# Kernel optimization log

Hardware: AMD Instinct MI355X
Metric: run time of the kernel (lower is better)

The kernel has to match this reference:

```python
import jax, jax.numpy as jnp
import numpy as np

B, T, D, H = 2, 2048, 1024, 16
DH = D // H
TOPK = 64


def setup_inputs() -> dict:
    key = jax.random.key(0)
    ks = jax.random.split(key, 10)
    s = D ** -0.5
    x = jax.random.normal(ks[0], (B, T, D), dtype=jnp.float32)
    key_padding_mask = jax.random.bernoulli(ks[1], 0.1, (B, T))
    Wq = jax.random.normal(ks[2], (D, D), dtype=jnp.float32) * s
    bq = jnp.zeros((D,), dtype=jnp.float32)
    Wk = jax.random.normal(ks[3], (D, D), dtype=jnp.float32) * s
    bk = jnp.zeros((D,), dtype=jnp.float32)
    Wv = jax.random.normal(ks[4], (D, D), dtype=jnp.float32) * s
    bv = jnp.zeros((D,), dtype=jnp.float32)
    Wo = jax.random.normal(ks[5], (D, D), dtype=jnp.float32) * s
    bo = jnp.zeros((D,), dtype=jnp.float32)
    return {"x": x, "Wq": Wq, "bq": bq, "Wk": Wk, "bk": bk,
            "Wv": Wv, "bv": bv, "Wo": Wo, "bo": bo,
            "key_padding_mask": key_padding_mask, "causal": 1}


def _attention(x, Wq, bq, Wk, bk, Wv, bv, Wo, bo, key_padding_mask, causal):
    b, t, d = x.shape
    dh = d // H

    def heads(y):  # (B,T,D) -> (B,H,T,Dh)
        return y.reshape(b, t, H, dh).transpose(0, 2, 1, 3)

    q = heads(x @ Wq.T + bq)
    k = heads(x @ Wk.T + bk)
    v = heads(x @ Wv.T + bv)

    scale = dh ** -0.5
    logits = jnp.einsum('bhqd,bhkd->bhqk', q, k) * scale  # (B,H,T,T)
    neg = jnp.finfo(logits.dtype).min

    # key padding mask: True blocks key position
    logits = jnp.where(key_padding_mask[:, None, None, :], neg, logits)

    if causal:
        i = jnp.arange(t)[:, None]
        j = jnp.arange(t)[None, :]
        blocked = j > (t - t + i)  # Tq == Tk
        logits = jnp.where(blocked[None, None], neg, logits)

    # hard top-k sparsification: keep top-k logits per row, rest -> -inf
    flat = logits.reshape(-1, t)  # (B*H*T, T)
    vals, idx = jax.lax.top_k(flat, TOPK)
    rows = jnp.arange(flat.shape[0])[:, None]
    sparse = jnp.full_like(flat, neg).at[rows, idx].set(vals)
    sparse = sparse.reshape(logits.shape)

    attn = jax.nn.softmax(sparse, axis=-1)
    out = jnp.einsum('bhqk,bhkd->bhqd', attn, v)  # (B,H,T,Dh)
    out = out.transpose(0, 2, 1, 3).reshape(b, t, d)
    return out @ Wo.T + bo


def reference(x, Wq, bq, Wk, bk, Wv, bv, Wo, bo, key_padding_mask, causal):
    return _attention(x, Wq, bq, Wk, bk, Wv, bv, Wo, bo, key_padding_mask, causal)
```

## Files before the change

kernel.cpp:

```cpp
#include <hip/hip_runtime.h>
#include <hip/hip_bf16.h>
#include <stdint.h>

#define BB 2
#define TT 2048
#define DD 1024
#define NH 16
#define HD 64
#define TOPK 64
#define NEGF (-3.402823466e38f)
#define ORD_NEG 0x00800000u
#define QT 16
#define KT 256
#define SELCAP 96

typedef short short8x __attribute__((ext_vector_type(8)));
typedef float floatx4 __attribute__((ext_vector_type(4)));

__device__ __forceinline__ uint32_t ord_u32(float x) {
    uint32_t b = __float_as_uint(x);
    return (b & 0x80000000u) ? ~b : (b | 0x80000000u);
}
__device__ __forceinline__ float unord(uint32_t u) {
    uint32_t b = (u & 0x80000000u) ? (u ^ 0x80000000u) : ~u;
    return __uint_as_float(b);
}
__device__ __forceinline__ short bf16_rne(float x) {
    uint32_t u = __float_as_uint(x);
    u += 0x7FFFu + ((u >> 16) & 1u);
    return (short)(u >> 16);
}
__device__ __forceinline__ float bf16_to_f(short h) {
    return __uint_as_float(((uint32_t)(uint16_t)h) << 16);
}
__device__ __forceinline__ bool mask_at(const void* m, int mode, int idx) {
    if (mode == 0) return ((const int*)m)[idx] != 0;
    if (mode == 1) return ((const unsigned char*)m)[idx] != 0;
    return ((const float*)m)[idx] != 0.0f;
}

__device__ __forceinline__ int dpp_wsum(int v) {
    v += __builtin_amdgcn_update_dpp(0, v, 0x111, 0xf, 0xf, true);
    v += __builtin_amdgcn_update_dpp(0, v, 0x112, 0xf, 0xf, true);
    v += __builtin_amdgcn_update_dpp(0, v, 0x114, 0xf, 0xf, true);
    v += __builtin_amdgcn_update_dpp(0, v, 0x118, 0xf, 0xf, true);
    v += __builtin_amdgcn_update_dpp(0, v, 0x142, 0xa, 0xf, true);
    v += __builtin_amdgcn_update_dpp(0, v, 0x143, 0xc, 0xf, true);
    return __builtin_amdgcn_readlane(v, 63);
}
__device__ __forceinline__ uint32_t dpp_wumax(uint32_t v) {
    uint32_t t;
    t = (uint32_t)__builtin_amdgcn_update_dpp(0, (int)v, 0x111, 0xf, 0xf, true); v = v > t ? v : t;
    t = (uint32_t)__builtin_amdgcn_update_dpp(0, (int)v, 0x112, 0xf, 0xf, true); v = v > t ? v : t;
    t = (uint32_t)__builtin_amdgcn_update_dpp(0, (int)v, 0x114, 0xf, 0xf, true); v = v > t ? v : t;
    t = (uint32_t)__builtin_amdgcn_update_dpp(0, (int)v, 0x118, 0xf, 0xf, true); v = v > t ? v : t;
    t = (uint32_t)__builtin_amdgcn_update_dpp(0, (int)v, 0x142, 0xa, 0xf, true); v = v > t ? v : t;
    t = (uint32_t)__builtin_amdgcn_update_dpp(0, (int)v, 0x143, 0xc, 0xf, true); v = v > t ? v : t;
    return (uint32_t)__builtin_amdgcn_readlane((int)v, 63);
}
__device__ __forceinline__ float dpp_fsum(float v) {
    v += __uint_as_float((uint32_t)__builtin_amdgcn_update_dpp(0, (int)__float_as_uint(v), 0x111, 0xf, 0xf, true));
    v += __uint_as_float((uint32_t)__builtin_amdgcn_update_dpp(0, (int)__float_as_uint(v), 0x112, 0xf, 0xf, true));
    v += __uint_as_float((uint32_t)__builtin_amdgcn_update_dpp(0, (int)__float_as_uint(v), 0x114, 0xf, 0xf, true));
    v += __uint_as_float((uint32_t)__builtin_amdgcn_update_dpp(0, (int)__float_as_uint(v), 0x118, 0xf, 0xf, true));
    v += __uint_as_float((uint32_t)__builtin_amdgcn_update_dpp(0, (int)__float_as_uint(v), 0x142, 0xa, 0xf, true));
    v += __uint_as_float((uint32_t)__builtin_amdgcn_update_dpp(0, (int)__float_as_uint(v), 0x143, 0xc, 0xf, true));
    return __uint_as_float((uint32_t)__builtin_amdgcn_readlane((int)__float_as_uint(v), 63));
}

__global__ void __launch_bounds__(1024) build_flags(
    const unsigned char* raw, const int* causalp, int* flags, uint32_t* Mt)
{
    __shared__ int odd_nz, big, s_mode;
    __shared__ uint32_t smt[BB * 64];
    const int tid = threadIdx.x;
    if (tid == 0) { odd_nz = 0; big = 0; }
    if (tid < BB * 64) smt[tid] = 0;
    __syncthreads();
    for (int i = tid; i < BB * TT; i += 1024) {
        unsigned char c = raw[i];
        if ((i & 3) && c) atomicOr(&odd_nz, 1);
        if (c > 1) atomicOr(&big, 1);
    }
    __syncthreads();
    if (tid == 0) {
        int mode = odd_nz ? (big ? 2 : 1) : 0;
        s_mode = mode;
        flags[0] = mode;
        flags[1] = (causalp[0] != 0) ? 1 : 0;
    }
    __syncthreads();
    const int mode = s_mode;
    const int w = tid >> 3, g = tid & 7;
    const int bb = w >> 6, l = w & 63;
    uint32_t bits = 0;
#pragma unroll
    for (int si = 0; si < 4; ++si) {
        int s = g * 4 + si;
        if (mask_at(raw, mode, bb * TT + l + 64 * s)) bits |= (1u << s);
    }
    if (bits) atomicOr(&smt[w], bits);
    __syncthreads();
    if (tid < BB * 64) Mt[tid] = smt[tid];
}

__global__ void __launch_bounds__(256) split_f32(
    const float* __restrict__ in, short* __restrict__ hi, short* __restrict__ lo,
    int n4, float scale)
{
    int i = blockIdx.x * blockDim.x + threadIdx.x;
    if (i >= n4) return;
    float4 v = ((const float4*)in)[i];
    float f[4] = {v.x * scale, v.y * scale, v.z * scale, v.w * scale};
    short hh[4], ll[4];
#pragma unroll
    for (int j = 0; j < 4; ++j) {
        hh[j] = bf16_rne(f[j]);
        ll[j] = bf16_rne(f[j] - bf16_to_f(hh[j]));
    }
    short4 h4; h4.x = hh[0]; h4.y = hh[1]; h4.z = hh[2]; h4.w = hh[3];
    short4 l4; l4.x = ll[0]; l4.y = ll[1]; l4.z = ll[2]; l4.w = ll[3];
    ((short4*)hi)[i] = h4;
    ((short4*)lo)[i] = l4;
}

__global__ void __launch_bounds__(256) split_w4(
    const float* __restrict__ W0, const float* __restrict__ W1,
    const float* __restrict__ W2, const float* __restrict__ W3,
    short* __restrict__ h0, short* __restrict__ l0, short* __restrict__ h1, short* __restrict__ l1,
    short* __restrict__ h2, short* __restrict__ l2, short* __restrict__ h3, short* __restrict__ l3,
    int n4)
{
    int i = blockIdx.x * blockDim.x + threadIdx.x;
    if (i >= n4) return;
    const int w = blockIdx.y;
    const float* in = (w == 0) ? W0 : (w == 1) ? W1 : (w == 2) ? W2 : W3;
    short* hi = (w == 0) ? h0 : (w == 1) ? h1 : (w == 2) ? h2 : h3;
    short* lo = (w == 0) ? l0 : (w == 1) ? l1 : (w == 2) ? l2 : l3;
    float4 v = ((const float4*)in)[i];
    float f[4] = {v.x, v.y, v.z, v.w};
    short hh[4], ll[4];
#pragma unroll
    for (int j = 0; j < 4; ++j) {
        hh[j] = bf16_rne(f[j]);
        ll[j] = bf16_rne(f[j] - bf16_to_f(hh[j]));
    }
    short4 h4; h4.x = hh[0]; h4.y = hh[1]; h4.z = hh[2]; h4.w = hh[3];
    short4 l4; l4.x = ll[0]; l4.y = ll[1]; l4.z = ll[2]; l4.w = ll[3];
    ((short4*)hi)[i] = h4;
    ((short4*)lo)[i] = l4;
}

__global__ void __launch_bounds__(256) gemm_bf16s(
    const short* __restrict__ Ah, const short* __restrict__ Al,
    const short* __restrict__ Bh, const short* __restrict__ Bl,
    const float* __restrict__ bias, float* __restrict__ Cf,
    short* __restrict__ Ch, short* __restrict__ Cl, float scale, int mode)
{
    const int bid = blockIdx.x;
    const int xcd = bid & 7, slot = bid >> 3;
    const int panel = xcd * 4 + (slot >> 4);
    const int ncol  = slot & 15;
    const int tid = threadIdx.x, lane = tid & 63, wv = tid >> 6;
    const int wr = wv >> 1, wc = wv & 1;
    const int m0 = panel * 128 + wr * 64;
    const int n0 = ncol * 64 + wc * 32;
    const int lrow = lane & 15, lk = (lane >> 4) * 8;

    floatx4 acc[4][2];
#pragma unroll
    for (int i = 0; i < 4; ++i)
#pragma unroll
        for (int j = 0; j < 2; ++j) acc[i][j] = (floatx4){0.f, 0.f, 0.f, 0.f};

    auto ldfr = [&](int kk, short8x* pah, short8x* pal, short8x* pbh, short8x* pbl) {
#pragma unroll
        for (int mb = 0; mb < 4; ++mb) {
            size_t off = (size_t)(m0 + mb * 16 + lrow) * DD + kk + lk;
            pah[mb] = *(const short8x*)(Ah + off);
            pal[mb] = *(const short8x*)(Al + off);
        }
#pragma unroll
        for (int nb = 0; nb < 2; ++nb) {
            size_t off = (size_t)(n0 + nb * 16 + lrow) * DD + kk + lk;
            pbh[nb] = *(const short8x*)(Bh + off);
            pbl[nb] = *(const short8x*)(Bl + off);
        }
    };
    auto domfma = [&](short8x* pah, short8x* pal, short8x* pbh, short8x* pbl) {
#pragma unroll
        for (int mb = 0; mb < 4; ++mb)
#pragma unroll
            for (int nb = 0; nb < 2; ++nb) {
                acc[mb][nb] = __builtin_amdgcn_mfma_f32_16x16x32_bf16(pah[mb], pbh[nb], acc[mb][nb], 0, 0, 0);
                acc[mb][nb] = __builtin_amdgcn_mfma_f32_16x16x32_bf16(pah[mb], pbl[nb], acc[mb][nb], 0, 0, 0);
                acc[mb][nb] = __builtin_amdgcn_mfma_f32_16x16x32_bf16(pal[mb], pbh[nb], acc[mb][nb], 0, 0, 0);
            }
    };

    short8x A0[4], L0[4], B0[2], C0[2];
    short8x A1[4], L1[4], B1[2], C1[2];
    ldfr(0, A0, L0, B0, C0);
    for (int kk = 0; kk < DD; kk += 64) {
        ldfr(kk + 32, A1, L1, B1, C1);
        domfma(A0, L0, B0, C0);
        if (kk + 64 < DD) ldfr(kk + 64, A0, L0, B0, C0);
        domfma(A1, L1, B1, C1);
    }

#pragma unroll
    for (int mb = 0; mb < 4; ++mb)
#pragma unroll
        for (int nb = 0; nb < 2; ++nb) {
            int n = n0 + nb * 16 + lrow;
            float bv = bias[n];
#pragma unroll
            for (int j = 0; j < 4; ++j) {
                int m = m0 + mb * 16 + (lane >> 4) * 4 + j;
                float v = acc[mb][nb][j] + bv;
                if (mode == 0) {
                    Cf[(size_t)m * DD + n] = v;
                } else {
                    int b = m >> 11, t = m & (TT - 1), h = n >> 6, dh = n & (HD - 1);
                    size_t idx = (((size_t)b * NH + h) * TT + t) * HD + dh;
                    if (mode == 1) {
                        Cf[idx] = v;
                    } else {
                        v *= scale;
                        short hi16 = bf16_rne(v);
                        Ch[idx] = hi16;
                        Cl[idx] = bf16_rne(v - bf16_to_f(hi16));
                    }
                }
            }
        }
}

__global__ void __launch_bounds__(256) gemm_xwt(
    const float* __restrict__ A, const float* __restrict__ W,
    const float* __restrict__ bias, float* __restrict__ C,
    int M, int N, int K, int split_heads)
{
    __shared__ float As[64][17];
    __shared__ float Ws[64][17];
    const int tid = threadIdx.x;
    const int tx = tid & 15, ty = tid >> 4;
    const int arow = blockIdx.y * 64, bcol = blockIdx.x * 64;
    float acc[4][4] = {};

    for (int k0 = 0; k0 < K; k0 += 16) {
        const int r = tid >> 2, c = (tid & 3) * 4;
        float4 a4 = *(const float4*)(A + (size_t)(arow + r) * K + k0 + c);
        As[r][c] = a4.x; As[r][c + 1] = a4.y; As[r][c + 2] = a4.z; As[r][c + 3] = a4.w;
        float4 w4 = *(const float4*)(W + (size_t)(bcol + r) * K + k0 + c);
        Ws[r][c] = w4.x; Ws[r][c + 1] = w4.y; Ws[r][c + 2] = w4.z; Ws[r][c + 3] = w4.w;
        __syncthreads();
#pragma unroll
        for (int k = 0; k < 16; ++k) {
            float a0 = As[ty * 4 + 0][k], a1 = As[ty * 4 + 1][k];
            float a2 = As[ty * 4 + 2][k], a3 = As[ty * 4 + 3][k];
            float w0 = Ws[tx * 4 + 0][k], w1 = Ws[tx * 4 + 1][k];
            float w2 = Ws[tx * 4 + 2][k], w3 = Ws[tx * 4 + 3][k];
            acc[0][0] += a0 * w0; acc[0][1] += a0 * w1; acc[0][2] += a0 * w2; acc[0][3] += a0 * w3;
            acc[1][0] += a1 * w0; acc[1][1] += a1 * w1; acc[1][2] += a1 * w2; acc[1][3] += a1 * w3;
            acc[2][0] += a2 * w0; acc[2][1] += a2 * w1; acc[2][2] += a2 * w2; acc[2][3] += a2 * w3;
            acc[3][0] += a3 * w0; acc[3][1] += a3 * w1; acc[3][2] += a3 * w2; acc[3][3] += a3 * w3;
        }
        __syncthreads();
    }

#pragma unroll
    for (int i = 0; i < 4; ++i) {
        int m = arow + ty * 4 + i;
#pragma unroll
        for (int j = 0; j < 4; ++j) {
            int n = bcol + tx * 4 + j;
            float v = acc[i][j] + bias[n];
            if (split_heads) {
                int b = m / TT, t = m % TT, h = n / HD, dh = n % HD;
                C[(((size_t)b * NH + h) * TT + t) * HD + dh] = v;
            } else {
                C[(size_t)m * N + n] = v;
            }
        }
    }
}

__global__ void __launch_bounds__(1024) attn_topk(
    const short* __restrict__ Qhi, const short* __restrict__ Qlo,
    const short* __restrict__ Khi, const short* __restrict__ Klo,
    const float* __restrict__ V, const uint32_t* __restrict__ Mt,
    const int* __restrict__ flags, short* __restrict__ Ohi,
    short* __restrict__ Olo, float* __restrict__ Of)
{
    __shared__ float s_S[2][QT][KT + 1];
    __shared__ int2  s_sel[QT][SELCAP];

    const int tid = threadIdx.x, lane = tid & 63, wv = tid >> 6;
    const int d = blockIdx.x;
    const int xcd = d & 7, chunk = d >> 3;
    const int bh = (xcd << 2) | (chunk >> 7);
    const int qt = chunk & 127;
    const int b = bh >> 4, h = bh & 15;
    const int causal = flags[1];
    const size_t hb = (size_t)bh * (size_t)TT * HD;
    const int r0 = qt * QT;
    const int gq = r0 + wv;
    const float* __restrict__ Vh = V + hb;
    const float* __restrict__ Vl = Vh + lane;

    short8x qhi[2], qlo[2];
    {
        const size_t qoff = hb + (size_t)(r0 + (lane & 15)) * HD + (lane >> 4) * 8;
        qhi[0] = *(const short8x*)(Qhi + qoff);
        qhi[1] = *(const short8x*)(Qhi + qoff + 32);
        qlo[0] = *(const short8x*)(Qlo + qoff);
        qlo[1] = *(const short8x*)(Qlo + qoff + 32);
    }

    const uint32_t mwords = Mt[b * 64 + lane];

    uint32_t lgo[32];
#pragma unroll
    for (int i = 0; i < 32; ++i) lgo[i] = ORD_NEG;

    const int lastT = causal ? ((r0 + QT - 1) >> 8) : 7;

#pragma unroll
    for (int t = 0; t < 8; ++t) {
        if (t <= lastT) {
            const size_t koff = hb + (size_t)(t * KT + wv * 16 + (lane & 15)) * HD + (lane >> 4) * 8;
            short8x kh0 = *(const short8x*)(Khi + koff);
            short8x kh1 = *(const short8x*)(Khi + koff + 32);
            short8x kl0 = *(const short8x*)(Klo + koff);
            short8x kl1 = *(const short8x*)(Klo + koff + 32);
            floatx4 acc = {0.f, 0.f, 0.f, 0.f};
            acc = __builtin_amdgcn_mfma_f32_16x16x32_bf16(qhi[0], kh0, acc, 0, 0, 0);
            acc = __builtin_amdgcn_mfma_f32_16x16x32_bf16(qhi[0], kl0, acc, 0, 0, 0);
            acc = __builtin_amdgcn_mfma_f32_16x16x32_bf16(qlo[0], kh0, acc, 0, 0, 0);
            acc = __builtin_amdgcn_mfma_f32_16x16x32_bf16(qhi[1], kh1, acc, 0, 0, 0);
            acc = __builtin_amdgcn_mfma_f32_16x16x32_bf16(qhi[1], kl1, acc, 0, 0, 0);
            acc = __builtin_amdgcn_mfma_f32_16x16x32_bf16(qlo[1], kh1, acc, 0, 0, 0);
#pragma unroll
            for (int j = 0; j < 4; ++j)
                s_S[t & 1][(lane >> 4) * 4 + j][wv * 16 + (lane & 15)] = acc[j];
            __syncthreads();
#pragma unroll
            for (int j = 0; j < 4; ++j) {
                float sv = s_S[t & 1][wv][j * 64 + lane];
                int key = t * KT + j * 64 + lane;
                bool blocked = ((mwords >> (t * 4 + j)) & 1u) || (causal && key > gq);
                lgo[t * 4 + j] = blocked ? ORD_NEG : ord_u32(sv);
            }
        }
    }

    uint32_t moL = 0;
#pragma unroll
    for (int i = 0; i < 32; ++i) {
        uint32_t u = lgo[i];
        moL = u > moL ? u : moL;
    }
    const uint32_t mo = dpp_wumax(moL);

    auto wcount = [&](uint32_t thrv) -> int {
        int c = 0;
#pragma unroll
        for (int i = 0; i < 32; ++i) c += (lgo[i] >= thrv) ? 1 : 0;
        return dpp_wsum(c);
    };

    float outv;
    if (mo == ORD_NEG) {
        float a0 = 0.f, a1 = 0.f, a2 = 0.f, a3 = 0.f;
        for (int j = 0; j < TT; j += 4) {
            a0 += Vh[(j + 0) * HD + lane];
            a1 += Vh[(j + 1) * HD + lane];
            a2 += Vh[(j + 2) * HD + lane];
            a3 += Vh[(j + 3) * HD + lane];
        }
        outv = (a0 + a1 + a2 + a3) * (1.0f / TT);
    } else {
        const float mF = unord(mo);
        uint32_t thr = 0; uint32_t lo_b = 0, hi_b = 0; int done = 0;
        {
            uint32_t p1 = ord_u32(mF - 2.0f);
            int c1 = wcount(p1);
            if (c1 == TOPK) { thr = p1; done = 1; }
            else if (c1 > TOPK) { lo_b = p1; hi_b = mo; }
            else {
                uint32_t p2 = ord_u32(mF - 4.0f);
                int c2 = wcount(p2);
                if (c2 == TOPK) { thr = p2; done = 1; }
                else if (c2 > TOPK) { lo_b = p2; hi_b = p1; }
                else {
                    uint32_t p3 = ord_u32(mF - 15.0f);
                    int c3 = wcount(p3);
                    if (c3 <= TOPK) { thr = p3; done = 1; }
                    else { lo_b = p3; hi_b = p2; }
                }
            }
        }
        if (!done) {
            while (hi_b - lo_b > 1u) {
                uint32_t mid = lo_b + ((hi_b - lo_b) >> 1);
                int c = wcount(mid);
                if (c == TOPK) { lo_b = mid; break; }
                if (c > TOPK) lo_b = mid; else hi_b = mid;
            }
            thr = lo_b;
        }

        float Sp = 0.f;
#pragma unroll
        for (int i = 0; i < 32; ++i) {
            uint32_t u = lgo[i];
            float w = 0.f;
            if (u >= thr) w = __expf(unord(u) - mF);
            Sp += w;
            lgo[i] = (w > 0.f) ? __float_as_uint(w) : 0u;
        }
        const float S = dpp_fsum(Sp);

        int base = 0;
#pragma unroll
        for (int i = 0; i < 32; ++i) {
            uint32_t wbits = lgo[i];
            unsigned long long msk = __ballot(wbits != 0);
            if (wbits) {
                int below = __builtin_amdgcn_mbcnt_hi((uint32_t)(msk >> 32),
                            __builtin_amdgcn_mbcnt_lo((uint32_t)msk, 0));
                int pos = base + below;
                if (pos < SELCAP) {
                    int keyoff = (((i >> 2) * KT + (i & 3) * 64 + lane) << 6);
                    s_sel[wv][pos] = make_int2(keyoff, (int)wbits);
                }
            }
            base += (int)__popcll(msk);
        }
        int cnt = base < SELCAP ? base : SELCAP;

        float acc = 0.f;
        int i2 = 0;
        for (; i2 + 4 <= cnt; i2 += 4) {
            int2 e0 = s_sel[wv][i2],     e1 = s_sel[wv][i2 + 1];
            int2 e2 = s_sel[wv][i2 + 2], e3 = s_sel[wv][i2 + 3];
            int k0 = __builtin_amdgcn_readfirstlane(e0.x);
            int k1 = __builtin_amdgcn_readfirstlane(e1.x);
            int k2 = __builtin_amdgcn_readfirstlane(e2.x);
            int k3 = __builtin_amdgcn_readfirstlane(e3.x);
            float w0 = __uint_as_float((uint32_t)__builtin_amdgcn_readfirstlane(e0.y));
            float w1 = __uint_as_float((uint32_t)__builtin_amdgcn_readfirstlane(e1.y));
            float w2 = __uint_as_float((uint32_t)__builtin_amdgcn_readfirstlane(e2.y));
            float w3 = __uint_as_float((uint32_t)__builtin_amdgcn_readfirstlane(e3.y));
            acc += w0 * Vl[k0];
            acc += w1 * Vl[k1];
            acc += w2 * Vl[k2];
            acc += w3 * Vl[k3];
        }
        for (; i2 < cnt; ++i2) {
            int2 e = s_sel[wv][i2];
            int k = __builtin_amdgcn_readfirstlane(e.x);
            float w = __uint_as_float((uint32_t)__builtin_amdgcn_readfirstlane(e.y));
            acc += w * Vl[k];
        }
        outv = acc / S;
    }
    const size_t oidx = ((size_t)b * TT + gq) * DD + h * HD + lane;
    if (Of) {
        Of[oidx] = outv;
    } else {
        short hi16 = bf16_rne(outv);
        Ohi[oidx] = hi16;
        Olo[oidx] = bf16_rne(outv - bf16_to_f(hi16));
    }
}

extern "C" void kernel_launch(void* const* d_in, const int* in_sizes, int n_in,
                              void* d_out, int out_size, void* d_ws, size_t ws_size,
                              hipStream_t stream) {
    const float* x  = (const float*)d_in[0];
    const float* Wq = (const float*)d_in[1];
    const float* bq = (const float*)d_in[2];
    const float* Wk = (const float*)d_in[3];
    const float* bk = (const float*)d_in[4];
    const float* Wv = (const float*)d_in[5];
    const float* bv = (const float*)d_in[6];
    const float* Wo = (const float*)d_in[7];
    const float* bo = (const float*)d_in[8];
    const void*  maskp = d_in[9];
    const int*   causalp = (const int*)d_in[10];
    float* out = (float*)d_out;

    char* ws = (char*)d_ws;
    const size_t TEN  = (size_t)BB * TT * DD * sizeof(float);
    const size_t HTEN = TEN / 2;
    const size_t WSZ  = (size_t)DD * DD * 2;
    const size_t NEED = 6 * TEN + 4096;

    const int nx4 = BB * TT * DD / 4, nw4 = DD * DD / 4;

    if (ws_size >= NEED) {
        float* Vf   = (float*)(ws);
        short* xh   = (short*)(ws + TEN);
        short* xl   = (short*)(ws + TEN + HTEN);
        short* Qhi  = (short*)(ws + 2 * TEN);
        short* Qlo  = (short*)(ws + 2 * TEN + HTEN);
        short* Khi  = (short*)(ws + 3 * TEN);
        short* Klo  = (short*)(ws + 3 * TEN + HTEN);
        short* Ohi  = (short*)(ws + 4 * TEN);
        short* Olo  = (short*)(ws + 4 * TEN + HTEN);
        char*  wb   = ws + 5 * TEN;
        short* wqh = (short*)(wb);            short* wql = (short*)(wb + WSZ);
        short* wkh = (short*)(wb + 2 * WSZ);  short* wkl = (short*)(wb + 3 * WSZ);
        short* wvh = (short*)(wb + 4 * WSZ);  short* wvl = (short*)(wb + 5 * WSZ);
        short* woh = (short*)(wb + 6 * WSZ);  short* wol = (short*)(wb + 7 * WSZ);
        int*      flags = (int*)(wb + 8 * WSZ);
        uint32_t* Mt    = (uint32_t*)(wb + 8 * WSZ + 256);

        build_flags<<<1, 1024, 0, stream>>>((const unsigned char*)maskp, causalp, flags, Mt);

        split_f32<<<(nx4 + 255) / 256, 256, 0, stream>>>(x, xh, xl, nx4, 1.0f);
        dim3 wg((nw4 + 255) / 256, 4);
        split_w4<<<wg, 256, 0, stream>>>(Wq, Wk, Wv, Wo,
                                         wqh, wql, wkh, wkl, wvh, wvl, woh, wol, nw4);

        gemm_bf16s<<<512, 256, 0, stream>>>(xh, xl, wqh, wql, bq, nullptr, Qhi, Qlo, 0.125f, 2);
        gemm_bf16s<<<512, 256, 0, stream>>>(xh, xl, wkh, wkl, bk, nullptr, Khi, Klo, 1.0f, 2);
        gemm_bf16s<<<512, 256, 0, stream>>>(xh, xl, wvh, wvl, bv, Vf, nullptr, nullptr, 1.0f, 1);

        attn_topk<<<BB * NH * (TT / QT), 1024, 0, stream>>>(Qhi, Qlo, Khi, Klo, Vf, Mt, flags,
                                                            Ohi, Olo, nullptr);

        gemm_bf16s<<<512, 256, 0, stream>>>(Ohi, Olo, woh, wol, bo, out, nullptr, nullptr, 1.0f, 0);
    } else {
        float* Qf  = (float*)(ws);
        float* Kf  = (float*)(ws + TEN);
        float* Vf  = (float*)(ws + 2 * TEN);
        float* O   = (float*)(ws + 3 * TEN);
        short* Qhi = (short*)(ws + 4 * TEN);
        short* Qlo = (short*)(ws + 4 * TEN + HTEN);
        short* Khi = (short*)(ws + 5 * TEN);
        short* Klo = (short*)(ws + 5 * TEN + HTEN);
        int*      flags = (int*)(ws + 6 * TEN);
        uint32_t* Mt    = (uint32_t*)(ws + 6 * TEN + 256);

        build_flags<<<1, 1024, 0, stream>>>((const unsigned char*)maskp, causalp, flags, Mt);
        dim3 g2(DD / 64, (BB * TT) / 64);
        gemm_xwt<<<g2, 256, 0, stream>>>(x, Wq, bq, Qf, BB * TT, DD, DD, 1);
        gemm_xwt<<<g2, 256, 0, stream>>>(x, Wk, bk, Kf, BB * TT, DD, DD, 1);
        gemm_xwt<<<g2, 256, 0, stream>>>(x, Wv, bv, Vf, BB * TT, DD, DD, 1);
        split_f32<<<(nx4 + 255) / 256, 256, 0, stream>>>(Qf, Qhi, Qlo, nx4, 0.125f);
        split_f32<<<(nx4 + 255) / 256, 256, 0, stream>>>(Kf, Khi, Klo, nx4, 1.0f);
        attn_topk<<<BB * NH * (TT / QT), 1024, 0, stream>>>(Qhi, Qlo, Khi, Klo, Vf, Mt, flags,
                                                            nullptr, nullptr, O);
        gemm_xwt<<<g2, 256, 0, stream>>>(O, Wo, bo, out, BB * TT, DD, DD, 0);
    }
}
```

Baseline: 770.4 us.

## Drop split-bf16 correction terms for V and output GEMMs; ballot-driven top-k gather

Adds a terms mask to the split-bf16 GEMM so the V projection and output projection run a single bf16 MFMA per tile instead of three. This removes the lo-part loads and extra MFMAs. The attention kernel no longer writes the O lo part, and its weighted V gather now walks ballot masks directly with readlane instead of compacting entries through shared memory. The cost is lower precision for V and the output, since both are now plain bf16, which risks tolerance failures.

```diff
diff --git a/kernel.cpp b/kernel.cpp
--- a/kernel.cpp
+++ b/kernel.cpp
@@ -12,7 +12,6 @@
 #define ORD_NEG 0x00800000u
 #define QT 16
 #define KT 256
-#define SELCAP 96
 
 typedef short short8x __attribute__((ext_vector_type(8)));
 typedef float floatx4 __attribute__((ext_vector_type(4)));
@@ -155,7 +154,7 @@
     const short* __restrict__ Ah, const short* __restrict__ Al,
     const short* __restrict__ Bh, const short* __restrict__ Bl,
     const float* __restrict__ bias, float* __restrict__ Cf,
-    short* __restrict__ Ch, short* __restrict__ Cl, float scale, int mode)
+    short* __restrict__ Ch, short* __restrict__ Cl, float scale, int mode, int terms)
 {
     const int bid = blockIdx.x;
     const int xcd = bid & 7, slot = bid >> 3;
@@ -178,13 +177,13 @@
         for (int mb = 0; mb < 4; ++mb) {
             size_t off = (size_t)(m0 + mb * 16 + lrow) * DD + kk + lk;
             pah[mb] = *(const short8x*)(Ah + off);
-            pal[mb] = *(const short8x*)(Al + off);
+            if (terms & 1) pal[mb] = *(const short8x*)(Al + off);
         }
 #pragma unroll
         for (int nb = 0; nb < 2; ++nb) {
             size_t off = (size_t)(n0 + nb * 16 + lrow) * DD + kk + lk;
             pbh[nb] = *(const short8x*)(Bh + off);
-            pbl[nb] = *(const short8x*)(Bl + off);
+            if (terms & 2) pbl[nb] = *(const short8x*)(Bl + off);
         }
     };
     auto domfma = [&](short8x* pah, short8x* pal, short8x* pbh, short8x* pbl) {
@@ -193,8 +192,10 @@
 #pragma unroll
             for (int nb = 0; nb < 2; ++nb) {
                 acc[mb][nb] = __builtin_amdgcn_mfma_f32_16x16x32_bf16(pah[mb], pbh[nb], acc[mb][nb], 0, 0, 0);
-                acc[mb][nb] = __builtin_amdgcn_mfma_f32_16x16x32_bf16(pah[mb], pbl[nb], acc[mb][nb], 0, 0, 0);
-                acc[mb][nb] = __builtin_amdgcn_mfma_f32_16x16x32_bf16(pal[mb], pbh[nb], acc[mb][nb], 0, 0, 0);
+                if (terms & 2)
+                    acc[mb][nb] = __builtin_amdgcn_mfma_f32_16x16x32_bf16(pah[mb], pbl[nb], acc[mb][nb], 0, 0, 0);
+                if (terms & 1)
+                    acc[mb][nb] = __builtin_amdgcn_mfma_f32_16x16x32_bf16(pal[mb], pbh[nb], acc[mb][nb], 0, 0, 0);
             }
     };
 
@@ -294,7 +295,6 @@
     short* __restrict__ Olo, float* __restrict__ Of)
 {
     __shared__ float s_S[2][QT][KT + 1];
-    __shared__ int2  s_sel[QT][SELCAP];
 
     const int tid = threadIdx.x, lane = tid & 63, wv = tid >> 6;
     const int d = blockIdx.x;
@@ -422,49 +422,23 @@
         }
         const float S = dpp_fsum(Sp);
 
-        int base = 0;
+        float a0 = 0.f, a1 = 0.f, a2 = 0.f, a3 = 0.f;
 #pragma unroll
         for (int i = 0; i < 32; ++i) {
-            uint32_t wbits = lgo[i];
-            unsigned long long msk = __ballot(wbits != 0);
-            if (wbits) {
-                int below = __builtin_amdgcn_mbcnt_hi((uint32_t)(msk >> 32),
-                            __builtin_amdgcn_mbcnt_lo((uint32_t)msk, 0));
-                int pos = base + below;
-                if (pos < SELCAP) {
-                    int keyoff = (((i >> 2) * KT + (i & 3) * 64 + lane) << 6);
-                    s_sel[wv][pos] = make_int2(keyoff, (int)wbits);
-                }
-            }
-            base += (int)__popcll(msk);
-        }
-        int cnt = base < SELCAP ? base : SELCAP;
-
-        float acc = 0.f;
-        int i2 = 0;
-        for (; i2 + 4 <= cnt; i2 += 4) {
-            int2 e0 = s_sel[wv][i2],     e1 = s_sel[wv][i2 + 1];
-            int2 e2 = s_sel[wv][i2 + 2], e3 = s_sel[wv][i2 + 3];
-            int k0 = __builtin_amdgcn_readfirstlane(e0.x);
-            int k1 = __builtin_amdgcn_readfirstlane(e1.x);
-            int k2 = __builtin_amdgcn_readfirstlane(e2.x);
-            int k3 = __builtin_amdgcn_readfirstlane(e3.x);
-            float w0 = __uint_as_float((uint32_t)__builtin_amdgcn_readfirstlane(e0.y));
-            float w1 = __uint_as_float((uint32_t)__builtin_amdgcn_readfirstlane(e1.y));
-            float w2 = __uint_as_float((uint32_t)__builtin_amdgcn_readfirstlane(e2.y));
-            float w3 = __uint_as_float((uint32_t)__builtin_amdgcn_readfirstlane(e3.y));
-            acc += w0 * Vl[k0];
-            acc += w1 * Vl[k1];
-            acc += w2 * Vl[k2];
-            acc += w3 * Vl[k3];
-        }
-        for (; i2 < cnt; ++i2) {
-            int2 e = s_sel[wv][i2];
-            int k = __builtin_amdgcn_readfirstlane(e.x);
-            float w = __uint_as_float((uint32_t)__builtin_amdgcn_readfirstlane(e.y));
-            acc += w * Vl[k];
-        }
-        outv = acc / S;
+            unsigned long long msk = __ballot(lgo[i] != 0u);
+            const int kbase = ((i >> 2) * KT + (i & 3) * 64) * HD;
+            while (msk) {
+                int src = (int)__builtin_ctzll(msk);
+                msk &= (msk - 1);
+                float w = __uint_as_float((uint32_t)__builtin_amdgcn_readlane((int)lgo[i], src));
+                float prod = w * Vl[kbase + src * HD];
+                if ((i & 3) == 0) a0 += prod;
+                else if ((i & 3) == 1) a1 += prod;
+                else if ((i & 3) == 2) a2 += prod;
+                else a3 += prod;
+            }
+        }
+        outv = ((a0 + a1) + (a2 + a3)) / S;
     }
     const size_t oidx = ((size_t)b * TT + gq) * DD + h * HD + lane;
     if (Of) {
@@ -472,7 +446,7 @@
     } else {
         short hi16 = bf16_rne(outv);
         Ohi[oidx] = hi16;
-        Olo[oidx] = bf16_rne(outv - bf16_to_f(hi16));
+        if (Olo) Olo[oidx] = bf16_rne(outv - bf16_to_f(hi16));
     }
 }
 
@@ -509,7 +483,6 @@
         short* Khi  = (short*)(ws + 3 * TEN);
         short* Klo  = (short*)(ws + 3 * TEN + HTEN);
         short* Ohi  = (short*)(ws + 4 * TEN);
-        short* Olo  = (short*)(ws + 4 * TEN + HTEN);
         char*  wb   = ws + 5 * TEN;
         short* wqh = (short*)(wb);            short* wql = (short*)(wb + WSZ);
         short* wkh = (short*)(wb + 2 * WSZ);  short* wkl = (short*)(wb + 3 * WSZ);
@@ -525,14 +498,14 @@
         split_w4<<<wg, 256, 0, stream>>>(Wq, Wk, Wv, Wo,
                                          wqh, wql, wkh, wkl, wvh, wvl, woh, wol, nw4);
 
-        gemm_bf16s<<<512, 256, 0, stream>>>(xh, xl, wqh, wql, bq, nullptr, Qhi, Qlo, 0.125f, 2);
-        gemm_bf16s<<<512, 256, 0, stream>>>(xh, xl, wkh, wkl, bk, nullptr, Khi, Klo, 1.0f, 2);
-        gemm_bf16s<<<512, 256, 0, stream>>>(xh, xl, wvh, wvl, bv, Vf, nullptr, nullptr, 1.0f, 1);
+        gemm_bf16s<<<512, 256, 0, stream>>>(xh, xl, wqh, wql, bq, nullptr, Qhi, Qlo, 0.125f, 2, 3);
+        gemm_bf16s<<<512, 256, 0, stream>>>(xh, xl, wkh, wkl, bk, nullptr, Khi, Klo, 1.0f, 2, 3);
+        gemm_bf16s<<<512, 256, 0, stream>>>(xh, xl, wvh, wvl, bv, Vf, nullptr, nullptr, 1.0f, 1, 0);
 
         attn_topk<<<BB * NH * (TT / QT), 1024, 0, stream>>>(Qhi, Qlo, Khi, Klo, Vf, Mt, flags,
-                                                            Ohi, Olo, nullptr);
-
-        gemm_bf16s<<<512, 256, 0, stream>>>(Ohi, Olo, woh, wol, bo, out, nullptr, nullptr, 1.0f, 0);
+                                                            Ohi, nullptr, nullptr);
+
+        gemm_bf16s<<<512, 256, 0, stream>>>(Ohi, Ohi, woh, wol, bo, out, nullptr, nullptr, 1.0f, 0, 0);
     } else {
         float* Qf  = (float*)(ws);
         float* Kf  = (float*)(ws + TEN);
```

Result: no change. 757.1 us (-1.7%).
